# Optimization experiments

Hardware: AMD Instinct MI355X
Metric: run time of the kernel (lower is better)

The kernel has to match this reference:

```python
import jax, jax.numpy as jnp
import numpy as np
import math

FACTOR = 1  # init kwarg

def setup_inputs() -> dict:
    key = jax.random.key(0)
    k1, k2 = jax.random.split(key)
    B, H, C, L = 32, 8, 64, 1024
    values = jax.random.normal(k1, (B, H, C, L), dtype=jnp.float32)
    corr = jax.random.uniform(k2, (B, H, C, L), dtype=jnp.float32)
    return {"values": values, "corr": corr}

def reference(values, corr):
    # Faithful translation of Auto_attn.time_delay_training.
    B, H, C, L = values.shape
    top_k = int(FACTOR * math.log(L))  # static: depends only on L
    # mean over head then channel -> [B, L]
    mean_value = corr.mean(axis=(1, 2))
    # top-k delays shared across the batch (argmax of batch-mean correlation)
    _, index = jax.lax.top_k(mean_value.mean(axis=0), top_k)  # [top_k]
    # per-batch weights at the selected delays -> [B, top_k]
    weights = mean_value[:, index]
    tmp_corr = jax.nn.softmax(weights, axis=-1)  # [B, top_k]
    # roll(values, -index[i], axis=-1) == gather at (t + index[i]) mod L
    gather_idx = (jnp.arange(L)[None, :] + index[:, None]) % L  # [top_k, L]
    pattern = jnp.take(values, gather_idx, axis=-1)  # [B, H, C, top_k, L]
    # softmax-weighted aggregation over the top_k delays
    delays_agg = jnp.einsum('bhckl,bk->bhcl', pattern, tmp_corr)
    return delays_agg
```

## Files before the change

### kernel.cpp

```cpp
#include <hip/hip_runtime.h>
#include <math.h>

#define B 32
#define H 8
#define C 64
#define L 1024
#define HC (H * C)
#define K 6
#define CHUNKS 32
#define ROWS_PER_CHUNK (HC / CHUNKS)

__global__ __launch_bounds__(256) void partial_sum_kernel(
    const float* __restrict__ corr, float* __restrict__ partial) {
    int blk = blockIdx.x;
    int b = blk / CHUNKS;
    int chunk = blk % CHUNKS;
    int tid = threadIdx.x;
    const float4* base =
        (const float4*)(corr + ((size_t)b * HC + (size_t)chunk * ROWS_PER_CHUNK) * L);
    float4 acc = make_float4(0.f, 0.f, 0.f, 0.f);
    for (int r = 0; r < ROWS_PER_CHUNK; ++r) {
        float4 v = base[r * (L / 4) + tid];
        acc.x += v.x; acc.y += v.y; acc.z += v.z; acc.w += v.w;
    }
    ((float4*)(partial + (size_t)blk * L))[tid] = acc;
}

__global__ __launch_bounds__(256) void mean_kernel(
    const float* __restrict__ partial, float* __restrict__ mean_value) {
    int gid = blockIdx.x * 256 + threadIdx.x;
    int b = gid / L;
    int l = gid - b * L;
    float s = 0.f;
    for (int c = 0; c < CHUNKS; ++c)
        s += partial[((size_t)b * CHUNKS + c) * L + l];
    mean_value[gid] = s * (1.0f / HC);
}

__global__ __launch_bounds__(1024) void topk_softmax_kernel(
    const float* __restrict__ mean_value,
    float* __restrict__ tmp_corr,
    int* __restrict__ index_out) {
    __shared__ float colmean[L];
    __shared__ float sval[1024];
    __shared__ int   sidx[1024];
    __shared__ int   sel[K];
    int t = threadIdx.x;

    float s = 0.f;
    for (int b = 0; b < B; ++b) s += mean_value[b * L + t];
    colmean[t] = s * (1.0f / B);
    __syncthreads();

    for (int k = 0; k < K; ++k) {
        sval[t] = colmean[t];
        sidx[t] = t;
        __syncthreads();
        for (int stride = 512; stride >= 1; stride >>= 1) {
            if (t < stride) {
                float v2 = sval[t + stride];
                int   i2 = sidx[t + stride];
                if (v2 > sval[t] || (v2 == sval[t] && i2 < sidx[t])) {
                    sval[t] = v2; sidx[t] = i2;
                }
            }
            __syncthreads();
        }
        if (t == 0) {
            sel[k] = sidx[0];
            colmean[sidx[0]] = -3.0e38f;
        }
        __syncthreads();
    }

    if (t < K) index_out[t] = sel[t];
    if (t < B) {
        float w[K];
        float m = -3.0e38f;
        for (int k = 0; k < K; ++k) {
            w[k] = mean_value[t * L + sel[k]];
            m = fmaxf(m, w[k]);
        }
        float sum = 0.f;
        for (int k = 0; k < K; ++k) { w[k] = expf(w[k] - m); sum += w[k]; }
        float inv = 1.0f / sum;
        for (int k = 0; k < K; ++k) tmp_corr[t * K + k] = w[k] * inv;
    }
}

__global__ __launch_bounds__(256) void agg_kernel(
    const float* __restrict__ values,
    const float* __restrict__ tmp_corr,
    const int* __restrict__ index,
    float* __restrict__ out) {
    __shared__ float row[L];
    __shared__ float w[K];
    __shared__ int   idx[K];
    int blk = blockIdx.x;
    int b = blk / HC;
    int tid = threadIdx.x;

    ((float4*)row)[tid] = ((const float4*)(values + (size_t)blk * L))[tid];
    if (tid < K) { w[tid] = tmp_corr[b * K + tid]; idx[tid] = index[tid]; }
    __syncthreads();

    int l0 = tid * 4;
    float4 acc = make_float4(0.f, 0.f, 0.f, 0.f);
    for (int k = 0; k < K; ++k) {
        float wk = w[k];
        int base = l0 + idx[k];
        acc.x += wk * row[(base + 0) & (L - 1)];
        acc.y += wk * row[(base + 1) & (L - 1)];
        acc.z += wk * row[(base + 2) & (L - 1)];
        acc.w += wk * row[(base + 3) & (L - 1)];
    }
    ((float4*)(out + (size_t)blk * L))[tid] = acc;
}

extern "C" void kernel_launch(void* const* d_in, const int* in_sizes, int n_in,
                              void* d_out, int out_size, void* d_ws, size_t ws_size,
                              hipStream_t stream) {
    const float* values = (const float*)d_in[0];
    const float* corr   = (const float*)d_in[1];
    float* out = (float*)d_out;

    float* partial    = (float*)d_ws;
    float* mean_value = partial + (size_t)B * CHUNKS * L;
    float* tmp_corr   = mean_value + (size_t)B * L;
    int*   index      = (int*)(tmp_corr + B * K);

    partial_sum_kernel<<<B * CHUNKS, 256, 0, stream>>>(corr, partial);
    mean_kernel<<<(B * L) / 256, 256, 0, stream>>>(partial, mean_value);
    topk_softmax_kernel<<<1, 1024, 0, stream>>>(mean_value, tmp_corr, index);
    agg_kernel<<<B * H * C, 256, 0, stream>>>(values, tmp_corr, index, out);
}
```

Before: 185.3 us.

## Use wave shuffles for top-k argmax and stride-1 LDS reads in aggregation

The top-k selection kernel now does its argmax with 64-lane xor shuffles and a small second stage across the 16 waves. This replaces the 10-step shared-memory tree reduction, which needed a barrier at every step. The aggregation kernel changes from four consecutive elements per thread (float4 store, strided LDS reads) to one element per thread across four 256-wide passes. That makes LDS reads and global stores contiguous across lanes and avoids bank conflicts, at the cost of scalar rather than vector stores.

```diff
diff --git a/kernel.cpp b/kernel.cpp
--- a/kernel.cpp
+++ b/kernel.cpp
@@ -41,36 +41,41 @@
     const float* __restrict__ mean_value,
     float* __restrict__ tmp_corr,
     int* __restrict__ index_out) {
-    __shared__ float colmean[L];
-    __shared__ float sval[1024];
-    __shared__ int   sidx[1024];
+    __shared__ float wval[16];
+    __shared__ int   widx[16];
     __shared__ int   sel[K];
     int t = threadIdx.x;
+    int lane = t & 63;
+    int wave = t >> 6;
 
     float s = 0.f;
     for (int b = 0; b < B; ++b) s += mean_value[b * L + t];
-    colmean[t] = s * (1.0f / B);
-    __syncthreads();
+    float cm = s * (1.0f / B);
+    int   ci = t;
 
     for (int k = 0; k < K; ++k) {
-        sval[t] = colmean[t];
-        sidx[t] = t;
+        float v = cm; int i = ci;
+        #pragma unroll
+        for (int off = 32; off >= 1; off >>= 1) {
+            float v2 = __shfl_xor(v, off, 64);
+            int   i2 = __shfl_xor(i, off, 64);
+            if (v2 > v || (v2 == v && i2 < i)) { v = v2; i = i2; }
+        }
+        if (lane == 0) { wval[wave] = v; widx[wave] = i; }
         __syncthreads();
-        for (int stride = 512; stride >= 1; stride >>= 1) {
-            if (t < stride) {
-                float v2 = sval[t + stride];
-                int   i2 = sidx[t + stride];
-                if (v2 > sval[t] || (v2 == sval[t] && i2 < sidx[t])) {
-                    sval[t] = v2; sidx[t] = i2;
-                }
+        if (wave == 0) {
+            float v3 = (lane < 16) ? wval[lane] : -3.0e38f;
+            int   i3 = (lane < 16) ? widx[lane] : 0x7fffffff;
+            #pragma unroll
+            for (int off = 8; off >= 1; off >>= 1) {
+                float v2 = __shfl_xor(v3, off, 64);
+                int   i2 = __shfl_xor(i3, off, 64);
+                if (v2 > v3 || (v2 == v3 && i2 < i3)) { v3 = v2; i3 = i2; }
             }
-            __syncthreads();
-        }
-        if (t == 0) {
-            sel[k] = sidx[0];
-            colmean[sidx[0]] = -3.0e38f;
+            if (lane == 0) sel[k] = i3;
         }
         __syncthreads();
+        if (ci == sel[k]) cm = -3.0e38f;
     }
 
     if (t < K) index_out[t] = sel[t];
@@ -94,27 +99,30 @@
     const int* __restrict__ index,
     float* __restrict__ out) {
     __shared__ float row[L];
-    __shared__ float w[K];
-    __shared__ int   idx[K];
+    __shared__ float ws[K];
+    __shared__ int   is[K];
     int blk = blockIdx.x;
     int b = blk / HC;
     int tid = threadIdx.x;
 
     ((float4*)row)[tid] = ((const float4*)(values + (size_t)blk * L))[tid];
-    if (tid < K) { w[tid] = tmp_corr[b * K + tid]; idx[tid] = index[tid]; }
+    if (tid < K) { ws[tid] = tmp_corr[b * K + tid]; is[tid] = index[tid]; }
     __syncthreads();
 
-    int l0 = tid * 4;
-    float4 acc = make_float4(0.f, 0.f, 0.f, 0.f);
-    for (int k = 0; k < K; ++k) {
-        float wk = w[k];
-        int base = l0 + idx[k];
-        acc.x += wk * row[(base + 0) & (L - 1)];
-        acc.y += wk * row[(base + 1) & (L - 1)];
-        acc.z += wk * row[(base + 2) & (L - 1)];
-        acc.w += wk * row[(base + 3) & (L - 1)];
+    float w[K]; int d[K];
+    #pragma unroll
+    for (int k = 0; k < K; ++k) { w[k] = ws[k]; d[k] = is[k]; }
+
+    float* orow = out + (size_t)blk * L;
+    #pragma unroll
+    for (int off = 0; off < L; off += 256) {
+        int l = tid + off;
+        float acc = 0.f;
+        #pragma unroll
+        for (int k = 0; k < K; ++k)
+            acc += w[k] * row[(l + d[k]) & (L - 1)];
+        orow[l] = acc;
     }
-    ((float4*)(out + (size_t)blk * L))[tid] = acc;
 }
 
 extern "C" void kernel_launch(void* const* d_in, const int* in_sizes, int n_in,
```

New measurement: 181.9 us. About the same (-1.9%).
